# Optimization experiments

Hardware: AMD Instinct MI355X
Metric: run time of the kernel (lower is better)

## Reference

```python
import jax, jax.numpy as jnp
import numpy as np

B, S, D, H = 2, 2048, 1024, 16
DH = D // H
SCALE = 1.0 / float(np.sqrt(DH))


def setup_inputs() -> dict:
    key = jax.random.key(0)
    ks = jax.random.split(key, 5)
    x = jax.random.normal(ks[0], (B, S, D), dtype=jnp.float32)
    init = 0.02
    Wq = jax.random.normal(ks[1], (D, D), dtype=jnp.float32) * init
    Wk = jax.random.normal(ks[2], (D, D), dtype=jnp.float32) * init
    Wv = jax.random.normal(ks[3], (D, D), dtype=jnp.float32) * init
    Wo = jax.random.normal(ks[4], (D, D), dtype=jnp.float32) * init
    bq = jnp.zeros((D,), dtype=jnp.float32)
    bk = jnp.zeros((D,), dtype=jnp.float32)
    bv = jnp.zeros((D,), dtype=jnp.float32)
    bo = jnp.zeros((D,), dtype=jnp.float32)
    return {"x": x, "Wq": Wq, "bq": bq, "Wk": Wk, "bk": bk,
            "Wv": Wv, "bv": bv, "Wo": Wo, "bo": bo}


def reference(x, Wq, bq, Wk, bk, Wv, bv, Wo, bo):
    # torch Linear: y = x @ W.T + b  (W: [out, in])
    q = x @ Wq.T + bq  # [B,S,D]
    k = x @ Wk.T + bk
    v = x @ Wv.T + bv
    # split heads -> [B,H,S,dh]
    q = q.reshape(B, S, H, DH).transpose(0, 2, 1, 3)
    k = k.reshape(B, S, H, DH).transpose(0, 2, 1, 3)
    v = v.reshape(B, S, H, DH).transpose(0, 2, 1, 3)
    scores = jnp.einsum('bhqd,bhkd->bhqk', q, k) * SCALE  # [B,H,S,S]
    p = jax.nn.softmax(scores, axis=-1)
    o = jnp.einsum('bhqk,bhkd->bhqd', p, v)  # [B,H,S,dh]
    # faithful to original: view(B, d_model, S) then transpose(-1,-2)
    o = o.reshape(B, D, S).swapaxes(-1, -2)  # [B,S,D]
    return o @ Wo.T + bo
```

## Files before the change

kernel.cpp:

```cpp
#include <hip/hip_runtime.h>
#include <cstdint>
#include <cstddef>


typedef _Float16 h16;
typedef _Float16 h16x8 __attribute__((ext_vector_type(8)));
typedef _Float16 h16x4 __attribute__((ext_vector_type(4)));
typedef _Float16 h16x2 __attribute__((ext_vector_type(2)));
typedef float    f32x4 __attribute__((ext_vector_type(4)));
typedef unsigned int u32x4 __attribute__((ext_vector_type(4)));

#define MFMA16 __builtin_amdgcn_mfma_f32_16x16x32_f16

#define QSCALE 0.1803368801111204f

#if __has_builtin(__builtin_amdgcn_exp2f)
#define EXP2F(x) __builtin_amdgcn_exp2f(x)
#else
#define EXP2F(x) exp2f(x)
#endif

__device__ __forceinline__ void gload_lds16(char* lds_dst, const void* gsrc) {
  __builtin_amdgcn_global_load_lds(
      (__attribute__((address_space(1))) void*)gsrc,
      (__attribute__((address_space(3))) void*)lds_dst,
      16, 0, 0);
}

__device__ __forceinline__ unsigned pk2(float lo, float hi) {
  return __builtin_bit_cast(unsigned, __builtin_amdgcn_cvt_pkrtz(lo, hi));
}

__device__ __forceinline__ float dot2a(unsigned p, float acc) {
#if __has_builtin(__builtin_amdgcn_fdot2)
  const h16x2 one = {(h16)1.f, (h16)1.f};
  return __builtin_amdgcn_fdot2(__builtin_bit_cast(h16x2, p), one, acc, false);
#else
  h16x2 v = __builtin_bit_cast(h16x2, p);
  return acc + (float)v[0] + (float)v[1];
#endif
}

__device__ __forceinline__ void swap32(unsigned& a, unsigned& b) {
  asm("v_permlane32_swap_b32 %0, %1" : "+v"(a), "+v"(b));
}

__device__ __forceinline__ h16x8 mk8(unsigned u0, unsigned u1, unsigned u2, unsigned u3) {
  u32x4 v = {u0, u1, u2, u3};
  return __builtin_bit_cast(h16x8, v);
}


__global__ __launch_bounds__(256)
void cast_all(const float* __restrict__ x,
              const float* __restrict__ wq, const float* __restrict__ wk,
              const float* __restrict__ wv, const float* __restrict__ wo,
              h16* __restrict__ xb, h16* __restrict__ wqb, h16* __restrict__ wkb,
              h16* __restrict__ wvb, h16* __restrict__ wob) {
  const int z = blockIdx.y;
  const float* src; h16* dst; int n4;
  switch (z) {
    case 0:  src = x;  dst = xb;  n4 = 1048576; break;
    case 1:  src = wq; dst = wqb; n4 = 262144;  break;
    case 2:  src = wk; dst = wkb; n4 = 262144;  break;
    case 3:  src = wv; dst = wvb; n4 = 262144;  break;
    default: src = wo; dst = wob; n4 = 262144;  break;
  }
  int i = blockIdx.x * 256 + threadIdx.x;
  const int stride = gridDim.x * 256;
  for (; i < n4; i += stride) {
    float4 v = reinterpret_cast<const float4*>(src)[i];
    h16x4 o = { (h16)v.x, (h16)v.y, (h16)v.z, (h16)v.w };
    reinterpret_cast<h16x4*>(dst)[i] = o;
  }
}

__device__ __forceinline__ void gemm_core_128(
    const h16* __restrict__ A, const h16* __restrict__ W,
    char* lds, f32x4 (&acc)[4][4])
{
  const int tid  = threadIdx.x;
  const int lane = tid & 63;
  const int w    = tid >> 6;
  const int wr   = w >> 1, wc = w & 1;
  const int blockRow = blockIdx.y * 128;
  const int blockCol = blockIdx.x * 128;

  const int sr  = (tid >> 2) & 15;
  const int sc  = tid & 3;
  const int skc = sc ^ ((sr >> 1) & 3);

  const h16* srcA0 = A + (size_t)(blockRow + (0 * 4 + w) * 16 + sr) * 1024 + skc * 8;
  const h16* srcA1 = A + (size_t)(blockRow + (1 * 4 + w) * 16 + sr) * 1024 + skc * 8;
  const h16* srcB0 = W + (size_t)(blockCol + (0 * 4 + w) * 16 + sr) * 1024 + skc * 8;
  const h16* srcB1 = W + (size_t)(blockCol + (1 * 4 + w) * 16 + sr) * 1024 + skc * 8;

  const int dA0o = w * 1024;
  const int dA1o = 4096 + w * 1024;
  const int dB0o = 8192 + w * 1024;
  const int dB1o = 12288 + w * 1024;

  const int fr = lane & 15, fg = lane >> 4;
  const int foff = fr * 64 + ((fg ^ ((fr >> 1) & 3)) << 4);

#pragma unroll
  for (int i = 0; i < 4; ++i)
#pragma unroll
    for (int j = 0; j < 4; ++j) acc[i][j] = f32x4{0.f, 0.f, 0.f, 0.f};

  gload_lds16(lds + dA0o, srcA0);
  gload_lds16(lds + dA1o, srcA1);
  gload_lds16(lds + dB0o, srcB0);
  gload_lds16(lds + dB1o, srcB1);

  for (int ks = 0; ks < 32; ++ks) {
    char* buf = lds + (ks & 1) * 16384;
    __syncthreads();
    if (ks != 31) {
      char* nbuf = lds + ((ks & 1) ^ 1) * 16384;
      gload_lds16(nbuf + dA0o, srcA0 + (ks + 1) * 32);
      gload_lds16(nbuf + dA1o, srcA1 + (ks + 1) * 32);
      gload_lds16(nbuf + dB0o, srcB0 + (ks + 1) * 32);
      gload_lds16(nbuf + dB1o, srcB1 + (ks + 1) * 32);
    }
    char* ldsA = buf;
    char* ldsB = buf + 8192;

    h16x8 af[4], bfv[4];
#pragma unroll
    for (int t = 0; t < 4; ++t)
      af[t] = *(const h16x8*)(ldsA + (wr * 4 + t) * 1024 + foff);
#pragma unroll
    for (int t = 0; t < 4; ++t)
      bfv[t] = *(const h16x8*)(ldsB + (wc * 4 + t) * 1024 + foff);
#pragma unroll
    for (int i = 0; i < 4; ++i)
#pragma unroll
      for (int j = 0; j < 4; ++j)
        acc[i][j] = MFMA16(af[i], bfv[j], acc[i][j], 0, 0, 0);
  }
}

__global__ __launch_bounds__(256, 2)
void gemm_qkv(const h16* __restrict__ xb,
              const h16* __restrict__ wq, const h16* __restrict__ wk, const h16* __restrict__ wv,
              const float* __restrict__ bq, const float* __restrict__ bk, const float* __restrict__ bv,
              h16* __restrict__ q_, h16* __restrict__ k_, h16* __restrict__ vt_)
{
  __shared__ alignas(128) char lds[32768];
  const int z = blockIdx.z;
  const h16* W = (z == 0) ? wq : (z == 1) ? wk : wv;
  const float* bias = (z == 0) ? bq : (z == 1) ? bk : bv;

  f32x4 acc[4][4];
  gemm_core_128(xb, W, lds, acc);

  const int lane = threadIdx.x & 63;
  const int w = threadIdx.x >> 6;
  const int wr = w >> 1, wc = w & 1;
  const int fr = lane & 15, fg = lane >> 4;
  const int blockRow = blockIdx.y * 128;
  const int blockCol = blockIdx.x * 128;

  if (z == 2) {
#pragma unroll
    for (int ct = 0; ct < 4; ++ct) {
      int n = blockCol + wc * 64 + ct * 16 + fr;
      int hh = n >> 6, dd = n & 63;
      float bv_ = bias[n];
#pragma unroll
      for (int rt = 0; rt < 4; ++rt) {
        int m = blockRow + wr * 64 + rt * 16 + 4 * fg;
        int bb = m >> 11, s0 = m & 2047;
        h16x4 pack = { (h16)(acc[rt][ct][0] + bv_), (h16)(acc[rt][ct][1] + bv_),
                       (h16)(acc[rt][ct][2] + bv_), (h16)(acc[rt][ct][3] + bv_) };
        *(h16x4*)(vt_ + ((size_t)((bb * 16 + hh) * 64 + dd)) * 2048 + s0) = pack;
      }
    }
  } else {
    const float scl = (z == 0) ? QSCALE : 1.0f;
    h16* dst = (z == 0) ? q_ : k_;
#pragma unroll
    for (int ct = 0; ct < 4; ++ct) {
      int n = blockCol + wc * 64 + ct * 16 + fr;
      float bv_ = bias[n];
#pragma unroll
      for (int rt = 0; rt < 4; ++rt) {
        int m0 = blockRow + wr * 64 + rt * 16 + 4 * fg;
#pragma unroll
        for (int r = 0; r < 4; ++r)
          dst[(size_t)(m0 + r) * 1024 + n] = (h16)((acc[rt][ct][r] + bv_) * scl);
      }
    }
  }
}

__global__ __launch_bounds__(256, 2)
void gemm_out(const h16* __restrict__ yt, const h16* __restrict__ wo,
              const float* __restrict__ bo, float* __restrict__ out)
{
  __shared__ alignas(128) char lds[32768];
  f32x4 acc[4][4];
  gemm_core_128(yt, wo, lds, acc);

  const int lane = threadIdx.x & 63;
  const int w = threadIdx.x >> 6;
  const int wr = w >> 1, wc = w & 1;
  const int fr = lane & 15, fg = lane >> 4;
  const int blockRow = blockIdx.y * 128;
  const int blockCol = blockIdx.x * 128;

#pragma unroll
  for (int ct = 0; ct < 4; ++ct) {
    int n = blockCol + wc * 64 + ct * 16 + fr;
    float bv_ = bo[n];
#pragma unroll
    for (int rt = 0; rt < 4; ++rt) {
      int m0 = blockRow + wr * 64 + rt * 16 + 4 * fg;
#pragma unroll
      for (int r = 0; r < 4; ++r)
        out[(size_t)(m0 + r) * 1024 + n] = acc[rt][ct][r] + bv_;
    }
  }
}

__global__ __launch_bounds__(256, 2)
void attn_kernel(const h16* __restrict__ qb, const h16* __restrict__ kb,
                 const h16* __restrict__ vtb, h16* __restrict__ ytb)
{
  __shared__ alignas(128) char lds[32768];
  const int tid = threadIdx.x, lane = tid & 63, w = tid >> 6;
  const int fr = lane & 15, fg = lane >> 4;

  const int orig = blockIdx.x;
  const int wgid = (orig & 7) * 64 + (orig >> 3);
  const int p  = wgid & 15;
  const int hh = (wgid >> 4) & 15;
  const int b  = wgid >> 8;

  const int aq = w * 16 + fr;
  const h16* qrowA = qb + ((size_t)(b * 2048 + 32 * aq + p)) * 1024 + hh * 64;
  const h16* qrowB = qrowA + 16 * 1024;
  h16x8 qfA0 = *(const h16x8*)(qrowA + fg * 8);
  h16x8 qfA1 = *(const h16x8*)(qrowA + 32 + fg * 8);
  h16x8 qfB0 = *(const h16x8*)(qrowB + fg * 8);
  h16x8 qfB1 = *(const h16x8*)(qrowB + 32 + fg * 8);

  const int sr  = (tid >> 2) & 15;
  const int sc  = tid & 3;
  const int skc = sc ^ ((sr >> 1) & 3);
  const int rloc0 = (w >> 1) * 16 + sr;
  const int rloc1 = ((4 + w) >> 1) * 16 + sr;
  const int kc0 = (w & 1) * 32 + skc * 8;
  const int kc1 = ((4 + w) & 1) * 32 + skc * 8;

  const h16* srcK0 = kb + ((size_t)(b * 2048 + rloc0)) * 1024 + hh * 64 + kc0;
  const h16* srcK1 = kb + ((size_t)(b * 2048 + rloc1)) * 1024 + hh * 64 + kc1;
  const h16* srcV0 = vtb + ((size_t)((b * 16 + hh) * 64 + rloc0)) * 2048 + kc0;
  const h16* srcV1 = vtb + ((size_t)((b * 16 + hh) * 64 + rloc1)) * 2048 + kc1;

  const int dK0o = w * 1024, dK1o = 4096 + w * 1024;
  const int dV0o = 8192 + w * 1024, dV1o = 12288 + w * 1024;

  const int foff = fr * 64 + ((fg ^ ((fr >> 1) & 3)) << 4);
  const int sfr  = (fr & 3) | ((fr & 4) << 1) | ((fr & 8) >> 1);
  const int foffK = sfr * 64 + ((fg ^ ((sfr >> 1) & 3)) << 4);

  f32x4 oA[4], oB[4];
#pragma unroll
  for (int i = 0; i < 4; ++i) { oA[i] = f32x4{0.f,0.f,0.f,0.f}; oB[i] = f32x4{0.f,0.f,0.f,0.f}; }
  float lA = 0.f, lB = 0.f;

  gload_lds16(lds + dK0o, srcK0);
  gload_lds16(lds + dK1o, srcK1);
  gload_lds16(lds + dV0o, srcV0);
  gload_lds16(lds + dV1o, srcV1);

  for (int ch = 0; ch < 32; ++ch) {
    char* buf = lds + (ch & 1) * 16384;
    __syncthreads();
    if (ch != 31) {
      char* nbuf = lds + ((ch & 1) ^ 1) * 16384;
      gload_lds16(nbuf + dK0o, srcK0 + (size_t)(ch + 1) * 65536);
      gload_lds16(nbuf + dK1o, srcK1 + (size_t)(ch + 1) * 65536);
      gload_lds16(nbuf + dV0o, srcV0 + (size_t)(ch + 1) * 64);
      gload_lds16(nbuf + dV1o, srcV1 + (size_t)(ch + 1) * 64);
    }
    char* ldsK = buf;
    char* ldsV = buf + 8192;

    unsigned pA[4][2], pB[4][2];
#pragma unroll
    for (int t = 0; t < 4; ++t) {
      h16x8 kf0 = *(const h16x8*)(ldsK + (t * 2 + 0) * 1024 + foffK);
      h16x8 kf1 = *(const h16x8*)(ldsK + (t * 2 + 1) * 1024 + foffK);
      f32x4 sA = f32x4{0.f,0.f,0.f,0.f};
      f32x4 sB = f32x4{0.f,0.f,0.f,0.f};
      __builtin_amdgcn_s_setprio(1);
      sA = MFMA16(kf0, qfA0, sA, 0, 0, 0);
      sA = MFMA16(kf1, qfA1, sA, 0, 0, 0);
      sB = MFMA16(kf0, qfB0, sB, 0, 0, 0);
      sB = MFMA16(kf1, qfB1, sB, 0, 0, 0);
      __builtin_amdgcn_s_setprio(0);
      pA[t][0] = pk2(EXP2F(sA[0]), EXP2F(sA[1]));
      pA[t][1] = pk2(EXP2F(sA[2]), EXP2F(sA[3]));
      pB[t][0] = pk2(EXP2F(sB[0]), EXP2F(sB[1]));
      pB[t][1] = pk2(EXP2F(sB[2]), EXP2F(sB[3]));
      lA = dot2a(pA[t][0], lA); lA = dot2a(pA[t][1], lA);
      lB = dot2a(pB[t][0], lB); lB = dot2a(pB[t][1], lB);
    }

    swap32(pA[0][0], pA[1][0]);  swap32(pA[0][1], pA[1][1]);
    swap32(pA[2][0], pA[3][0]);  swap32(pA[2][1], pA[3][1]);
    swap32(pB[0][0], pB[1][0]);  swap32(pB[0][1], pB[1][1]);
    swap32(pB[2][0], pB[3][0]);  swap32(pB[2][1], pB[3][1]);
    h16x8 pfA0 = mk8(pA[0][0], pA[0][1], pA[1][0], pA[1][1]);
    h16x8 pfA1 = mk8(pA[2][0], pA[2][1], pA[3][0], pA[3][1]);
    h16x8 pfB0 = mk8(pB[0][0], pB[0][1], pB[1][0], pB[1][1]);
    h16x8 pfB1 = mk8(pB[2][0], pB[2][1], pB[3][0], pB[3][1]);

    __builtin_amdgcn_s_setprio(1);
#pragma unroll
    for (int dt = 0; dt < 4; ++dt) {
      h16x8 vf0 = *(const h16x8*)(ldsV + (dt * 2 + 0) * 1024 + foff);
      h16x8 vf1 = *(const h16x8*)(ldsV + (dt * 2 + 1) * 1024 + foff);
      oA[dt] = MFMA16(pfA0, vf0, oA[dt], 0, 0, 0);
      oA[dt] = MFMA16(pfA1, vf1, oA[dt], 0, 0, 0);
      oB[dt] = MFMA16(pfB0, vf0, oB[dt], 0, 0, 0);
      oB[dt] = MFMA16(pfB1, vf1, oB[dt], 0, 0, 0);
    }
    __builtin_amdgcn_s_setprio(0);
  }

  lA += __shfl_xor(lA, 16); lA += __shfl_xor(lA, 32);
  lB += __shfl_xor(lB, 16); lB += __shfl_xor(lB, 32);
  float iA = 1.0f / lA, iB = 1.0f / lB;
  float iAr[4], iBr[4];
#pragma unroll
  for (int r = 0; r < 4; ++r) {
    int src = (lane & 48) | (4 * fg + r);
    iAr[r] = __shfl(iA, src);
    iBr[r] = __shfl(iB, src);
  }

#pragma unroll
  for (int dt = 0; dt < 4; ++dt) {
    int row = dt * 16 + fr;
    size_t colb = (size_t)(hh * 64 + w * 16 + fg * 4);
    h16x4 sA4 = { (h16)(oA[dt][0] * iAr[0]), (h16)(oA[dt][1] * iAr[1]),
                  (h16)(oA[dt][2] * iAr[2]), (h16)(oA[dt][3] * iAr[3]) };
    h16x4 sB4 = { (h16)(oB[dt][0] * iBr[0]), (h16)(oB[dt][1] * iBr[1]),
                  (h16)(oB[dt][2] * iBr[2]), (h16)(oB[dt][3] * iBr[3]) };
    *(h16x4*)(ytb + ((size_t)(b * 2048 + p * 64 + row)) * 1024 + colb) = sA4;
    *(h16x4*)(ytb + ((size_t)(b * 2048 + (p + 16) * 64 + row)) * 1024 + colb) = sB4;
  }
}

extern "C" void kernel_launch(void* const* d_in, const int* in_sizes, int n_in,
                              void* d_out, int out_size, void* d_ws, size_t ws_size,
                              hipStream_t stream) {
  const float* x  = (const float*)d_in[0];
  const float* Wq = (const float*)d_in[1];
  const float* bq = (const float*)d_in[2];
  const float* Wk = (const float*)d_in[3];
  const float* bk = (const float*)d_in[4];
  const float* Wv = (const float*)d_in[5];
  const float* bv = (const float*)d_in[6];
  const float* Wo = (const float*)d_in[7];
  const float* bo = (const float*)d_in[8];

  char* ws = (char*)d_ws;
  h16* xb  = (h16*)(ws);
  h16* wqb = (h16*)(ws + (size_t)(8  << 20));
  h16* wkb = (h16*)(ws + (size_t)(10 << 20));
  h16* wvb = (h16*)(ws + (size_t)(12 << 20));
  h16* wob = (h16*)(ws + (size_t)(14 << 20));
  h16* q_  = (h16*)(ws + (size_t)(16 << 20));
  h16* k_  = (h16*)(ws + (size_t)(24 << 20));
  h16* vt_ = (h16*)(ws + (size_t)(32 << 20));
  h16* yt_ = (h16*)(ws + (size_t)(40 << 20));

  cast_all<<<dim3(512, 5), 256, 0, stream>>>(x, Wq, Wk, Wv, Wo, xb, wqb, wkb, wvb, wob);
  gemm_qkv<<<dim3(8, 32, 3), 256, 0, stream>>>(xb, wqb, wkb, wvb, bq, bk, bv, q_, k_, vt_);
  attn_kernel<<<512, 256, 0, stream>>>(q_, k_, vt_, yt_);
  gemm_out<<<dim3(8, 32, 1), 256, 0, stream>>>(yt_, wob, bo, (float*)d_out);
}
```

Measured before the change: 106.8 us.

## Double attention KV chunk to 128 keys and compute row sums via MFMA

The attention loop now processes 128 keys per iteration instead of 64, halving the number of barriers and async load rounds and doubling the LDS footprint to 64 KB. The softmax denominator is accumulated with an extra MFMA against a ones vector, replacing the per-element dot2 adds and the final cross-lane shuffles. The larger LDS use may cut occupancy below the two workgroups per CU requested in launch bounds. The higher register pressure from the 8x2 probability arrays may also cause spills.

```diff
diff --git a/kernel.cpp b/kernel.cpp
--- a/kernel.cpp
+++ b/kernel.cpp
@@ -29,16 +29,6 @@
 
 __device__ __forceinline__ unsigned pk2(float lo, float hi) {
   return __builtin_bit_cast(unsigned, __builtin_amdgcn_cvt_pkrtz(lo, hi));
-}
-
-__device__ __forceinline__ float dot2a(unsigned p, float acc) {
-#if __has_builtin(__builtin_amdgcn_fdot2)
-  const h16x2 one = {(h16)1.f, (h16)1.f};
-  return __builtin_amdgcn_fdot2(__builtin_bit_cast(h16x2, p), one, acc, false);
-#else
-  h16x2 v = __builtin_bit_cast(h16x2, p);
-  return acc + (float)v[0] + (float)v[1];
-#endif
 }
 
 __device__ __forceinline__ void swap32(unsigned& a, unsigned& b) {
@@ -228,7 +218,7 @@
 void attn_kernel(const h16* __restrict__ qb, const h16* __restrict__ kb,
                  const h16* __restrict__ vtb, h16* __restrict__ ytb)
 {
-  __shared__ alignas(128) char lds[32768];
+  __shared__ alignas(128) char lds[65536];
   const int tid = threadIdx.x, lane = tid & 63, w = tid >> 6;
   const int fr = lane & 15, fg = lane >> 4;
 
@@ -249,49 +239,57 @@
   const int sr  = (tid >> 2) & 15;
   const int sc  = tid & 3;
   const int skc = sc ^ ((sr >> 1) & 3);
-  const int rloc0 = (w >> 1) * 16 + sr;
-  const int rloc1 = ((4 + w) >> 1) * 16 + sr;
-  const int kc0 = (w & 1) * 32 + skc * 8;
-  const int kc1 = ((4 + w) & 1) * 32 + skc * 8;
-
-  const h16* srcK0 = kb + ((size_t)(b * 2048 + rloc0)) * 1024 + hh * 64 + kc0;
-  const h16* srcK1 = kb + ((size_t)(b * 2048 + rloc1)) * 1024 + hh * 64 + kc1;
-  const h16* srcV0 = vtb + ((size_t)((b * 16 + hh) * 64 + rloc0)) * 2048 + kc0;
-  const h16* srcV1 = vtb + ((size_t)((b * 16 + hh) * 64 + rloc1)) * 2048 + kc1;
-
-  const int dK0o = w * 1024, dK1o = 4096 + w * 1024;
-  const int dV0o = 8192 + w * 1024, dV1o = 12288 + w * 1024;
+
+  const h16* srcK[4]; const h16* srcV[4];
+  int dK[4], dV[4];
+#pragma unroll
+  for (int i = 0; i < 4; ++i) {
+    int su = 4 * i + w;
+    int krow = (su >> 1) * 16 + sr;
+    int kcol = (su & 1) * 32 + skc * 8;
+    srcK[i] = kb + ((size_t)(b * 2048 + krow)) * 1024 + hh * 64 + kcol;
+    dK[i] = su * 1024;
+    int vrow = (su >> 2) * 16 + sr;
+    int vcol = (su & 3) * 32 + skc * 8;
+    srcV[i] = vtb + ((size_t)((b * 16 + hh) * 64 + vrow)) * 2048 + vcol;
+    dV[i] = 16384 + su * 1024;
+  }
 
   const int foff = fr * 64 + ((fg ^ ((fr >> 1) & 3)) << 4);
   const int sfr  = (fr & 3) | ((fr & 4) << 1) | ((fr & 8) >> 1);
   const int foffK = sfr * 64 + ((fg ^ ((sfr >> 1) & 3)) << 4);
 
+  const h16x8 ones8 = { (h16)1.f, (h16)1.f, (h16)1.f, (h16)1.f,
+                        (h16)1.f, (h16)1.f, (h16)1.f, (h16)1.f };
+
   f32x4 oA[4], oB[4];
 #pragma unroll
   for (int i = 0; i < 4; ++i) { oA[i] = f32x4{0.f,0.f,0.f,0.f}; oB[i] = f32x4{0.f,0.f,0.f,0.f}; }
-  float lA = 0.f, lB = 0.f;
-
-  gload_lds16(lds + dK0o, srcK0);
-  gload_lds16(lds + dK1o, srcK1);
-  gload_lds16(lds + dV0o, srcV0);
-  gload_lds16(lds + dV1o, srcV1);
-
-  for (int ch = 0; ch < 32; ++ch) {
-    char* buf = lds + (ch & 1) * 16384;
+  f32x4 lA4 = f32x4{0.f,0.f,0.f,0.f}, lB4 = f32x4{0.f,0.f,0.f,0.f};
+
+#pragma unroll
+  for (int i = 0; i < 4; ++i) {
+    gload_lds16(lds + dK[i], srcK[i]);
+    gload_lds16(lds + dV[i], srcV[i]);
+  }
+
+  for (int ch = 0; ch < 16; ++ch) {
+    char* buf = lds + (ch & 1) * 32768;
     __syncthreads();
-    if (ch != 31) {
-      char* nbuf = lds + ((ch & 1) ^ 1) * 16384;
-      gload_lds16(nbuf + dK0o, srcK0 + (size_t)(ch + 1) * 65536);
-      gload_lds16(nbuf + dK1o, srcK1 + (size_t)(ch + 1) * 65536);
-      gload_lds16(nbuf + dV0o, srcV0 + (size_t)(ch + 1) * 64);
-      gload_lds16(nbuf + dV1o, srcV1 + (size_t)(ch + 1) * 64);
+    if (ch != 15) {
+      char* nbuf = lds + ((ch & 1) ^ 1) * 32768;
+#pragma unroll
+      for (int i = 0; i < 4; ++i) {
+        gload_lds16(nbuf + dK[i], srcK[i] + (size_t)(ch + 1) * 131072);
+        gload_lds16(nbuf + dV[i], srcV[i] + (size_t)(ch + 1) * 128);
+      }
     }
     char* ldsK = buf;
-    char* ldsV = buf + 8192;
-
-    unsigned pA[4][2], pB[4][2];
-#pragma unroll
-    for (int t = 0; t < 4; ++t) {
+    char* ldsV = buf + 16384;
+
+    unsigned pA[8][2], pB[8][2];
+#pragma unroll
+    for (int t = 0; t < 8; ++t) {
       h16x8 kf0 = *(const h16x8*)(ldsK + (t * 2 + 0) * 1024 + foffK);
       h16x8 kf1 = *(const h16x8*)(ldsK + (t * 2 + 1) * 1024 + foffK);
       f32x4 sA = f32x4{0.f,0.f,0.f,0.f};
@@ -306,51 +304,50 @@
       pA[t][1] = pk2(EXP2F(sA[2]), EXP2F(sA[3]));
       pB[t][0] = pk2(EXP2F(sB[0]), EXP2F(sB[1]));
       pB[t][1] = pk2(EXP2F(sB[2]), EXP2F(sB[3]));
-      lA = dot2a(pA[t][0], lA); lA = dot2a(pA[t][1], lA);
-      lB = dot2a(pB[t][0], lB); lB = dot2a(pB[t][1], lB);
-    }
-
-    swap32(pA[0][0], pA[1][0]);  swap32(pA[0][1], pA[1][1]);
-    swap32(pA[2][0], pA[3][0]);  swap32(pA[2][1], pA[3][1]);
-    swap32(pB[0][0], pB[1][0]);  swap32(pB[0][1], pB[1][1]);
-    swap32(pB[2][0], pB[3][0]);  swap32(pB[2][1], pB[3][1]);
-    h16x8 pfA0 = mk8(pA[0][0], pA[0][1], pA[1][0], pA[1][1]);
-    h16x8 pfA1 = mk8(pA[2][0], pA[2][1], pA[3][0], pA[3][1]);
-    h16x8 pfB0 = mk8(pB[0][0], pB[0][1], pB[1][0], pB[1][1]);
-    h16x8 pfB1 = mk8(pB[2][0], pB[2][1], pB[3][0], pB[3][1]);
+    }
+
+#pragma unroll
+    for (int qd = 0; qd < 4; ++qd) {
+      swap32(pA[2*qd][0], pA[2*qd+1][0]);  swap32(pA[2*qd][1], pA[2*qd+1][1]);
+      swap32(pB[2*qd][0], pB[2*qd+1][0]);  swap32(pB[2*qd][1], pB[2*qd+1][1]);
+    }
+    h16x8 pfA[4], pfB[4];
+#pragma unroll
+    for (int qd = 0; qd < 4; ++qd) {
+      pfA[qd] = mk8(pA[2*qd][0], pA[2*qd][1], pA[2*qd+1][0], pA[2*qd+1][1]);
+      pfB[qd] = mk8(pB[2*qd][0], pB[2*qd][1], pB[2*qd+1][0], pB[2*qd+1][1]);
+    }
 
     __builtin_amdgcn_s_setprio(1);
 #pragma unroll
+    for (int j = 0; j < 4; ++j) {
+      lA4 = MFMA16(pfA[j], ones8, lA4, 0, 0, 0);
+      lB4 = MFMA16(pfB[j], ones8, lB4, 0, 0, 0);
+    }
+#pragma unroll
     for (int dt = 0; dt < 4; ++dt) {
-      h16x8 vf0 = *(const h16x8*)(ldsV + (dt * 2 + 0) * 1024 + foff);
-      h16x8 vf1 = *(const h16x8*)(ldsV + (dt * 2 + 1) * 1024 + foff);
-      oA[dt] = MFMA16(pfA0, vf0, oA[dt], 0, 0, 0);
-      oA[dt] = MFMA16(pfA1, vf1, oA[dt], 0, 0, 0);
-      oB[dt] = MFMA16(pfB0, vf0, oB[dt], 0, 0, 0);
-      oB[dt] = MFMA16(pfB1, vf1, oB[dt], 0, 0, 0);
+#pragma unroll
+      for (int j = 0; j < 4; ++j) {
+        h16x8 vf = *(const h16x8*)(ldsV + (dt * 4 + j) * 1024 + foff);
+        oA[dt] = MFMA16(pfA[j], vf, oA[dt], 0, 0, 0);
+        oB[dt] = MFMA16(pfB[j], vf, oB[dt], 0, 0, 0);
+      }
     }
     __builtin_amdgcn_s_setprio(0);
   }
 
-  lA += __shfl_xor(lA, 16); lA += __shfl_xor(lA, 32);
-  lB += __shfl_xor(lB, 16); lB += __shfl_xor(lB, 32);
-  float iA = 1.0f / lA, iB = 1.0f / lB;
-  float iAr[4], iBr[4];
-#pragma unroll
-  for (int r = 0; r < 4; ++r) {
-    int src = (lane & 48) | (4 * fg + r);
-    iAr[r] = __shfl(iA, src);
-    iBr[r] = __shfl(iB, src);
-  }
+  f32x4 iA4, iB4;
+#pragma unroll
+  for (int r = 0; r < 4; ++r) { iA4[r] = 1.0f / lA4[r]; iB4[r] = 1.0f / lB4[r]; }
 
 #pragma unroll
   for (int dt = 0; dt < 4; ++dt) {
     int row = dt * 16 + fr;
     size_t colb = (size_t)(hh * 64 + w * 16 + fg * 4);
-    h16x4 sA4 = { (h16)(oA[dt][0] * iAr[0]), (h16)(oA[dt][1] * iAr[1]),
-                  (h16)(oA[dt][2] * iAr[2]), (h16)(oA[dt][3] * iAr[3]) };
-    h16x4 sB4 = { (h16)(oB[dt][0] * iBr[0]), (h16)(oB[dt][1] * iBr[1]),
-                  (h16)(oB[dt][2] * iBr[2]), (h16)(oB[dt][3] * iBr[3]) };
+    h16x4 sA4 = { (h16)(oA[dt][0] * iA4[0]), (h16)(oA[dt][1] * iA4[1]),
+                  (h16)(oA[dt][2] * iA4[2]), (h16)(oA[dt][3] * iA4[3]) };
+    h16x4 sB4 = { (h16)(oB[dt][0] * iB4[0]), (h16)(oB[dt][1] * iB4[1]),
+                  (h16)(oB[dt][2] * iB4[2]), (h16)(oB[dt][3] * iB4[3]) };
     *(h16x4*)(ytb + ((size_t)(b * 2048 + p * 64 + row)) * 1024 + colb) = sA4;
     *(h16x4*)(ytb + ((size_t)(b * 2048 + (p + 16) * 64 + row)) * 1024 + colb) = sB4;
   }
```

Result: no change. 107.1 us (+0.3%).

## Split attention KV range across two workgroups and merge partial outputs

Applied to the files above, without the earlier changes.

Each attention workgroup now covers half the key/value sequence, doubling the grid to 1024 blocks and raising the occupancy hint to 4. Unnormalized partial outputs and row sums go to separate buffers, and a new merge kernel adds them and normalizes. Row sums are now computed with an MFMA against a ones vector instead of dot2 accumulation. This aims to fill the GPU's compute units better, at the cost of an extra launch, partial output traffic, and a strided gather of the sums in the merge kernel.

```diff
diff --git a/kernel.cpp b/kernel.cpp
--- a/kernel.cpp
+++ b/kernel.cpp
@@ -29,16 +29,6 @@
 
 __device__ __forceinline__ unsigned pk2(float lo, float hi) {
   return __builtin_bit_cast(unsigned, __builtin_amdgcn_cvt_pkrtz(lo, hi));
-}
-
-__device__ __forceinline__ float dot2a(unsigned p, float acc) {
-#if __has_builtin(__builtin_amdgcn_fdot2)
-  const h16x2 one = {(h16)1.f, (h16)1.f};
-  return __builtin_amdgcn_fdot2(__builtin_bit_cast(h16x2, p), one, acc, false);
-#else
-  h16x2 v = __builtin_bit_cast(h16x2, p);
-  return acc + (float)v[0] + (float)v[1];
-#endif
 }
 
 __device__ __forceinline__ void swap32(unsigned& a, unsigned& b) {
@@ -224,19 +214,26 @@
   }
 }
 
-__global__ __launch_bounds__(256, 2)
+__global__ __launch_bounds__(256, 4)
 void attn_kernel(const h16* __restrict__ qb, const h16* __restrict__ kb,
-                 const h16* __restrict__ vtb, h16* __restrict__ ytb)
+                 const h16* __restrict__ vtb,
+                 h16* __restrict__ o1, h16* __restrict__ o2,
+                 float* __restrict__ l1, float* __restrict__ l2)
 {
   __shared__ alignas(128) char lds[32768];
   const int tid = threadIdx.x, lane = tid & 63, w = tid >> 6;
   const int fr = lane & 15, fg = lane >> 4;
 
   const int orig = blockIdx.x;
-  const int wgid = (orig & 7) * 64 + (orig >> 3);
-  const int p  = wgid & 15;
-  const int hh = (wgid >> 4) & 15;
-  const int b  = wgid >> 8;
+  const int wgid = (orig & 7) * 128 + (orig >> 3);
+  const int half = wgid & 1;
+  const int p    = (wgid >> 1) & 15;
+  const int hh   = (wgid >> 5) & 15;
+  const int b    = wgid >> 9;
+  const int kvb  = half * 1024;
+
+  h16* __restrict__ oP = half ? o2 : o1;
+  float* __restrict__ lP = half ? l2 : l1;
 
   const int aq = w * 16 + fr;
   const h16* qrowA = qb + ((size_t)(b * 2048 + 32 * aq + p)) * 1024 + hh * 64;
@@ -254,10 +251,10 @@
   const int kc0 = (w & 1) * 32 + skc * 8;
   const int kc1 = ((4 + w) & 1) * 32 + skc * 8;
 
-  const h16* srcK0 = kb + ((size_t)(b * 2048 + rloc0)) * 1024 + hh * 64 + kc0;
-  const h16* srcK1 = kb + ((size_t)(b * 2048 + rloc1)) * 1024 + hh * 64 + kc1;
-  const h16* srcV0 = vtb + ((size_t)((b * 16 + hh) * 64 + rloc0)) * 2048 + kc0;
-  const h16* srcV1 = vtb + ((size_t)((b * 16 + hh) * 64 + rloc1)) * 2048 + kc1;
+  const h16* srcK0 = kb + ((size_t)(b * 2048 + kvb + rloc0)) * 1024 + hh * 64 + kc0;
+  const h16* srcK1 = kb + ((size_t)(b * 2048 + kvb + rloc1)) * 1024 + hh * 64 + kc1;
+  const h16* srcV0 = vtb + ((size_t)((b * 16 + hh) * 64 + rloc0)) * 2048 + kvb + kc0;
+  const h16* srcV1 = vtb + ((size_t)((b * 16 + hh) * 64 + rloc1)) * 2048 + kvb + kc1;
 
   const int dK0o = w * 1024, dK1o = 4096 + w * 1024;
   const int dV0o = 8192 + w * 1024, dV1o = 12288 + w * 1024;
@@ -266,20 +263,23 @@
   const int sfr  = (fr & 3) | ((fr & 4) << 1) | ((fr & 8) >> 1);
   const int foffK = sfr * 64 + ((fg ^ ((sfr >> 1) & 3)) << 4);
 
+  const h16x8 ones8 = { (h16)1.f, (h16)1.f, (h16)1.f, (h16)1.f,
+                        (h16)1.f, (h16)1.f, (h16)1.f, (h16)1.f };
+
   f32x4 oA[4], oB[4];
 #pragma unroll
   for (int i = 0; i < 4; ++i) { oA[i] = f32x4{0.f,0.f,0.f,0.f}; oB[i] = f32x4{0.f,0.f,0.f,0.f}; }
-  float lA = 0.f, lB = 0.f;
+  f32x4 lA4 = f32x4{0.f,0.f,0.f,0.f}, lB4 = f32x4{0.f,0.f,0.f,0.f};
 
   gload_lds16(lds + dK0o, srcK0);
   gload_lds16(lds + dK1o, srcK1);
   gload_lds16(lds + dV0o, srcV0);
   gload_lds16(lds + dV1o, srcV1);
 
-  for (int ch = 0; ch < 32; ++ch) {
+  for (int ch = 0; ch < 16; ++ch) {
     char* buf = lds + (ch & 1) * 16384;
     __syncthreads();
-    if (ch != 31) {
+    if (ch != 15) {
       char* nbuf = lds + ((ch & 1) ^ 1) * 16384;
       gload_lds16(nbuf + dK0o, srcK0 + (size_t)(ch + 1) * 65536);
       gload_lds16(nbuf + dK1o, srcK1 + (size_t)(ch + 1) * 65536);
@@ -306,8 +306,6 @@
       pA[t][1] = pk2(EXP2F(sA[2]), EXP2F(sA[3]));
       pB[t][0] = pk2(EXP2F(sB[0]), EXP2F(sB[1]));
       pB[t][1] = pk2(EXP2F(sB[2]), EXP2F(sB[3]));
-      lA = dot2a(pA[t][0], lA); lA = dot2a(pA[t][1], lA);
-      lB = dot2a(pB[t][0], lB); lB = dot2a(pB[t][1], lB);
     }
 
     swap32(pA[0][0], pA[1][0]);  swap32(pA[0][1], pA[1][1]);
@@ -320,6 +318,10 @@
     h16x8 pfB1 = mk8(pB[2][0], pB[2][1], pB[3][0], pB[3][1]);
 
     __builtin_amdgcn_s_setprio(1);
+    lA4 = MFMA16(pfA0, ones8, lA4, 0, 0, 0);
+    lA4 = MFMA16(pfA1, ones8, lA4, 0, 0, 0);
+    lB4 = MFMA16(pfB0, ones8, lB4, 0, 0, 0);
+    lB4 = MFMA16(pfB1, ones8, lB4, 0, 0, 0);
 #pragma unroll
     for (int dt = 0; dt < 4; ++dt) {
       h16x8 vf0 = *(const h16x8*)(ldsV + (dt * 2 + 0) * 1024 + foff);
@@ -332,28 +334,49 @@
     __builtin_amdgcn_s_setprio(0);
   }
 
-  lA += __shfl_xor(lA, 16); lA += __shfl_xor(lA, 32);
-  lB += __shfl_xor(lB, 16); lB += __shfl_xor(lB, 32);
-  float iA = 1.0f / lA, iB = 1.0f / lB;
-  float iAr[4], iBr[4];
-#pragma unroll
-  for (int r = 0; r < 4; ++r) {
-    int src = (lane & 48) | (4 * fg + r);
-    iAr[r] = __shfl(iA, src);
-    iBr[r] = __shfl(iB, src);
-  }
-
 #pragma unroll
   for (int dt = 0; dt < 4; ++dt) {
     int row = dt * 16 + fr;
     size_t colb = (size_t)(hh * 64 + w * 16 + fg * 4);
-    h16x4 sA4 = { (h16)(oA[dt][0] * iAr[0]), (h16)(oA[dt][1] * iAr[1]),
-                  (h16)(oA[dt][2] * iAr[2]), (h16)(oA[dt][3] * iAr[3]) };
-    h16x4 sB4 = { (h16)(oB[dt][0] * iBr[0]), (h16)(oB[dt][1] * iBr[1]),
-                  (h16)(oB[dt][2] * iBr[2]), (h16)(oB[dt][3] * iBr[3]) };
-    *(h16x4*)(ytb + ((size_t)(b * 2048 + p * 64 + row)) * 1024 + colb) = sA4;
-    *(h16x4*)(ytb + ((size_t)(b * 2048 + (p + 16) * 64 + row)) * 1024 + colb) = sB4;
-  }
+    h16x4 sA4 = { (h16)oA[dt][0], (h16)oA[dt][1], (h16)oA[dt][2], (h16)oA[dt][3] };
+    h16x4 sB4 = { (h16)oB[dt][0], (h16)oB[dt][1], (h16)oB[dt][2], (h16)oB[dt][3] };
+    *(h16x4*)(oP + ((size_t)(b * 2048 + p * 64 + row)) * 1024 + colb) = sA4;
+    *(h16x4*)(oP + ((size_t)(b * 2048 + (p + 16) * 64 + row)) * 1024 + colb) = sB4;
+  }
+  if (fr == 0) {
+    float* lb_ = lP + ((size_t)(b * 16 + hh)) * 2048;
+#pragma unroll
+    for (int r = 0; r < 4; ++r) {
+      int a = w * 16 + fg * 4 + r;
+      lb_[32 * a + p]      = lA4[r];
+      lb_[32 * a + p + 16] = lB4[r];
+    }
+  }
+}
+
+__global__ __launch_bounds__(256)
+void merge_halves(const h16* __restrict__ o1, const h16* __restrict__ o2,
+                  const float* __restrict__ l1, const float* __restrict__ l2,
+                  h16* __restrict__ yt)
+{
+  int idx = blockIdx.x * 256 + threadIdx.x;
+  int row  = idx >> 7;
+  int colg = (idx & 127) << 3;
+  int b  = row >> 11;
+  int b2 = (row >> 6) & 31;
+  int h  = colg >> 6;
+  int a0 = colg & 63;
+  const float* L1 = l1 + ((size_t)(b * 16 + h)) * 2048 + b2;
+  const float* L2 = l2 + ((size_t)(b * 16 + h)) * 2048 + b2;
+  h16x8 u1 = *(const h16x8*)(o1 + (size_t)row * 1024 + colg);
+  h16x8 u2 = *(const h16x8*)(o2 + (size_t)row * 1024 + colg);
+  h16x8 yv;
+#pragma unroll
+  for (int i = 0; i < 8; ++i) {
+    float inv = 1.0f / (L1[32 * (a0 + i)] + L2[32 * (a0 + i)]);
+    yv[i] = (h16)(((float)u1[i] + (float)u2[i]) * inv);
+  }
+  *(h16x8*)(yt + (size_t)row * 1024 + colg) = yv;
 }
 
 extern "C" void kernel_launch(void* const* d_in, const int* in_sizes, int n_in,
@@ -378,10 +401,15 @@
   h16* q_  = (h16*)(ws + (size_t)(16 << 20));
   h16* k_  = (h16*)(ws + (size_t)(24 << 20));
   h16* vt_ = (h16*)(ws + (size_t)(32 << 20));
-  h16* yt_ = (h16*)(ws + (size_t)(40 << 20));
+  h16* o1_ = (h16*)(ws + (size_t)(40 << 20));
+  h16* o2_ = (h16*)(ws + (size_t)(48 << 20));
+  float* l1_ = (float*)(ws + (size_t)(56 << 20));
+  float* l2_ = (float*)(ws + (size_t)(56 << 20) + 262144);
+  h16* yt_ = (h16*)(ws);
 
   cast_all<<<dim3(512, 5), 256, 0, stream>>>(x, Wq, Wk, Wv, Wo, xb, wqb, wkb, wvb, wob);
   gemm_qkv<<<dim3(8, 32, 3), 256, 0, stream>>>(xb, wqb, wkb, wvb, bq, bk, bv, q_, k_, vt_);
-  attn_kernel<<<512, 256, 0, stream>>>(q_, k_, vt_, yt_);
+  attn_kernel<<<1024, 256, 0, stream>>>(q_, k_, vt_, o1_, o2_, l1_, l2_);
+  merge_halves<<<2048, 256, 0, stream>>>(o1_, o2_, l1_, l2_, yt_);
   gemm_out<<<dim3(8, 32, 1), 256, 0, stream>>>(yt_, wob, bo, (float*)d_out);
 }
```

Result: slower. 141.7 us (+32.7%).
